# Optimization experiments

Hardware: AMD Instinct MI355X
Metric: run time of the kernel (lower is better)

The kernel has to match this reference:

```python
import jax, jax.numpy as jnp
import numpy as np

N = 50000
E = 800000
D = 128
EPS = 1e-5


def setup_inputs() -> dict:
    key = jax.random.key(0)
    ks = jax.random.split(key, 8)
    scale = 1.0 / np.sqrt(D)
    x = jax.random.normal(ks[0], (N, D), dtype=jnp.float32)
    edge_index = jax.random.randint(ks[1], (2, E), 0, N, dtype=jnp.int64)
    return {
        "x": x,
        "edge_index": edge_index,
        "W1l": jax.random.normal(ks[2], (D, D), dtype=jnp.float32) * scale,
        "b1": jnp.zeros((D,), jnp.float32),
        "W1r": jax.random.normal(ks[3], (D, D), dtype=jnp.float32) * scale,
        "g1": jnp.ones((D,), jnp.float32),
        "bt1": jnp.zeros((D,), jnp.float32),
        "W2l": jax.random.normal(ks[4], (D, D), dtype=jnp.float32) * scale,
        "b2": jnp.zeros((D,), jnp.float32),
        "W2r": jax.random.normal(ks[5], (D, D), dtype=jnp.float32) * scale,
        "g2": jnp.ones((D,), jnp.float32),
        "bt2": jnp.zeros((D,), jnp.float32),
    }


def _sage(x, src, dst, Wl, b, Wr):
    # mean aggregation of source features at destination nodes
    agg = jax.ops.segment_sum(x[src], dst, num_segments=N)  # [N, D]
    deg = jax.ops.segment_sum(jnp.ones((E,), x.dtype), dst, num_segments=N)
    agg = agg / jnp.maximum(deg, 1.0)[:, None]
    # PyG SAGEConv: lin_l(agg) + bias + lin_r(x) (root, no bias)
    return agg @ Wl + b + x @ Wr


def _bn(h, g, bt):
    # training-mode batch norm over node dim
    mu = jnp.mean(h, axis=0)
    var = jnp.var(h, axis=0)
    return (h - mu) * (g / jnp.sqrt(var + EPS)) + bt


def reference(x, edge_index, W1l, b1, W1r, g1, bt1, W2l, b2, W2r, g2, bt2):
    src, dst = edge_index[0], edge_index[1]
    h = _sage(x, src, dst, W1l, b1, W1r)
    h = jax.nn.relu(_bn(h, g1, bt1))
    # dropout = identity (eval mode)
    h = _sage(h, src, dst, W2l, b2, W2r)
    h = _bn(h, g2, bt2)
    # residual (in_channels == out_channels -> identity skip)
    return jax.nn.relu(h + x)
```

## Files before the change

kernel.cpp:

```cpp
#include <hip/hip_runtime.h>

typedef unsigned short u16;
typedef unsigned char u8;
typedef __attribute__((ext_vector_type(8))) short short8;
typedef __attribute__((ext_vector_type(2))) float f32x2;
typedef __attribute__((ext_vector_type(4))) float f32x4;
typedef __attribute__((ext_vector_type(4))) int i32x4;
typedef __attribute__((ext_vector_type(4))) unsigned short us4;
typedef __attribute__((ext_vector_type(8))) unsigned short us8;
typedef __attribute__((ext_vector_type(4))) unsigned int u32x4;

#define N_NODES 50000
#define N_EDGES 800000
#define DIM 128
#define NINV (1.0f / 50000.0f)
#define SROW 136
#define NBKT 3125
#define CAP 512
#define SUPN 800
#define NSUP 63
#define SEGCAP 16384

__device__ __forceinline__ float bf2f(u16 u) {
    union { unsigned int i; float f; } v; v.i = ((unsigned int)u) << 16; return v.f;
}
__device__ __forceinline__ u16 f2bf(float f) {
    union { float f; unsigned int i; } v; v.f = f;
    return (u16)((v.i + 0x7FFFu + ((v.i >> 16) & 1u)) >> 16);
}

__global__ __launch_bounds__(256) void k_prep(
        const float* __restrict__ W1l, const float* __restrict__ W1r, u16* __restrict__ Bp1,
        const float* __restrict__ W2l, const float* __restrict__ W2r, u16* __restrict__ Bp2,
        const float* __restrict__ x, u16* __restrict__ xh, u8* __restrict__ xf8,
        const int* __restrict__ esrc, const int* __restrict__ edst,
        int* __restrict__ segCnt, unsigned* __restrict__ segBuf, int splitB) {
    int b = blockIdx.x;
    if (b < 32) {
        const float* Wl = (b < 16) ? W1l : W2l;
        const float* Wr = (b < 16) ? W1r : W2r;
        u16* Bp = (b < 16) ? Bp1 : Bp2;
        int idx = (b & 15) * 256 + threadIdx.x;
        int lane = idx & 63;
        int kc = (idx >> 6) & 7;
        int nt = idx >> 9;
        int q = lane >> 4, nn = lane & 15;
        int col = nt * 16 + nn;
        #pragma unroll
        for (int j = 0; j < 8; ++j) {
            int k = kc * 32 + q * 8 + j;
            float v = (k < 128) ? Wl[k * 128 + col] : Wr[(k - 128) * 128 + col];
            Bp[(long)idx * 8 + j] = f2bf(v);
        }
    } else if (b < 32 + splitB) {
        long i4 = ((long)(b - 32) * 256 + threadIdx.x) * 4;
        f32x4 v = *(const f32x4*)(x + i4);
        us4 h;
        #pragma unroll
        for (int j = 0; j < 4; ++j) h[j] = f2bf(v[j]);
        *(us4*)(xh + i4) = h;
        int p = __builtin_amdgcn_cvt_pk_fp8_f32(v[0], v[1], 0, false);
        p = __builtin_amdgcn_cvt_pk_fp8_f32(v[2], v[3], p, true);
        *(int*)(xf8 + i4) = p;
    } else {
        __shared__ int sHistB[64], sScanB[64], sCurB[64], sBaseB[64];
        __shared__ unsigned sStage[1024];
        __shared__ u8 sBinOf[1024];
        int tid = threadIdx.x;
        int hb = b - 32 - splitB;
        int e4 = hb * 1024 + tid * 4;
        bool val = e4 < N_EDGES;
        if (tid < 64) sHistB[tid] = 0;
        __syncthreads();
        unsigned ent[4]; int bin[4];
        if (val) {
            i32x4 d4 = *(const i32x4*)(edst + e4);
            i32x4 s4 = *(const i32x4*)(esrc + e4);
            #pragma unroll
            for (int j = 0; j < 4; ++j) {
                unsigned dd = (unsigned)d4[j];
                int bi = (int)(dd / 800u);
                bin[j] = bi;
                ent[j] = ((unsigned)s4[j] << 10) | (dd - (unsigned)bi * 800u);
                atomicAdd(&sHistB[bi], 1);
            }
        }
        __syncthreads();
        if (tid == 0) {
            int acc = 0;
            #pragma unroll
            for (int i = 0; i < 64; ++i) { sScanB[i] = acc; sCurB[i] = acc; acc += sHistB[i]; }
        }
        __syncthreads();
        if (val) {
            #pragma unroll
            for (int j = 0; j < 4; ++j) {
                int p = atomicAdd(&sCurB[bin[j]], 1);
                sStage[p] = ent[j];
                sBinOf[p] = (u8)bin[j];
            }
        }
        __syncthreads();
        if (tid < 64) {
            int c = sHistB[tid];
            sBaseB[tid] = c ? atomicAdd(&segCnt[tid << 4], c) : 0;
        }
        __syncthreads();
        int tcount = sScanB[63] + sHistB[63];
        for (int p = tid; p < tcount; p += 256) {
            int bn = sBinOf[p];
            long ofs = (long)sBaseB[bn] + (p - sScanB[bn]);
            if (ofs < SEGCAP)
                segBuf[(long)bn * SEGCAP + ofs] = sStage[p];
        }
    }
}

__global__ __launch_bounds__(512) void k_sort(
        const int* __restrict__ segCnt, const unsigned* __restrict__ segBuf,
        u16* __restrict__ col_srt, u16* __restrict__ hdr) {
    __shared__ int sHist[SUPN], sStart[SUPN], sCur[SUPN];
    int tid = threadIdx.x;
    int s = blockIdx.x;
    int nnodes = N_NODES - s * SUPN; if (nnodes > SUPN) nnodes = SUPN;
    int ngroups = nnodes >> 4;
    int n = segCnt[s << 4]; if (n > SEGCAP) n = SEGCAP;
    for (int i = tid; i < SUPN; i += 512) { sHist[i] = 0; sCur[i] = 0; }
    __syncthreads();
    const unsigned* seg = segBuf + (long)s * SEGCAP;
    unsigned ent[32];
    #pragma unroll
    for (int i = 0; i < 32; ++i) {
        int idx = i * 512 + tid;
        ent[i] = (idx < n) ? seg[idx] : 0xFFFFFFFFu;
    }
    #pragma unroll
    for (int i = 0; i < 32; ++i)
        if (ent[i] != 0xFFFFFFFFu) atomicAdd(&sHist[ent[i] & 1023u], 1);
    __syncthreads();
    if (tid < ngroups) {
        int base = 0;
        int gb = (s * 50 + tid) * 32;
        #pragma unroll
        for (int i = 0; i < 16; ++i) {
            int node = tid * 16 + i;
            int d = sHist[node];
            int st_c = base < CAP ? base : CAP;
            int en_c = base + d < CAP ? base + d : CAP;
            sStart[node] = base;
            hdr[gb + i] = (u16)st_c;
            hdr[gb + 16 + i] = (u16)(en_c - st_c);
            base += d;
        }
    }
    __syncthreads();
    #pragma unroll
    for (int i = 0; i < 32; ++i) {
        unsigned e = ent[i];
        if (e != 0xFFFFFFFFu) {
            int node = (int)(e & 1023u);
            int pos = atomicAdd(&sCur[node], 1);
            int ofs = sStart[node] + pos;
            if (ofs < CAP)
                col_srt[(long)(s * 50 + (node >> 4)) * CAP + ofs] = (u16)(e >> 10);
        }
    }
}

template<int BN>
__device__ __forceinline__ void acc_row16(u32x4 w,
        float sum[16], const float av[16], const float ov[16]) {
    float t[16];
    f32x2 p;
    #pragma unroll
    for (int h = 0; h < 4; ++h) {
        p = __builtin_amdgcn_cvt_pk_f32_fp8((int)w[h], false); t[h*4+0] = p[0]; t[h*4+1] = p[1];
        p = __builtin_amdgcn_cvt_pk_f32_fp8((int)w[h], true);  t[h*4+2] = p[0]; t[h*4+3] = p[1];
    }
    #pragma unroll
    for (int k = 0; k < 16; ++k) {
        float v = t[k];
        if (BN) { v = v * av[k] + ov[k]; v = v > 0.f ? v : 0.f; }
        sum[k] += v;
    }
}

template<int BN, int W8>
__global__ __launch_bounds__(256) void k_ag(
        const u8* __restrict__ fq, const u16* __restrict__ fh,
        const u16* __restrict__ hdr, const u16* __restrict__ col_srt,
        const u16* __restrict__ Bph, const float* __restrict__ bias,
        const float* __restrict__ statsPrev, const float* __restrict__ gP,
        const float* __restrict__ btP,
        u16* __restrict__ h16, u8* __restrict__ h8, float* __restrict__ stats) {
    __shared__ u16 sA[16 * SROW];
    __shared__ float acS[256];
    __shared__ __align__(16) u16 sIdx[CAP];
    int tid = threadIdx.x;
    long nodebase = (long)blockIdx.x * 16;

    if (tid < 64)
        *(us8*)(sIdx + tid * 8) = *(const us8*)(col_srt + (long)blockIdx.x * CAP + tid * 8);

    if (BN) {
        if (tid < 128) {
            float s = 0.f, qq = 0.f;
            #pragma unroll
            for (int b = 0; b < 8; ++b) {
                s  += statsPrev[b * 512 + tid];
                qq += statsPrev[b * 512 + 256 + tid];
            }
            float mu = s * NINV;
            float var = qq * NINV - mu * mu;
            float a = gP[tid] * rsqrtf(var + 1e-5f);
            acS[tid] = a;
            acS[128 + tid] = btP[tid] - mu * a;
        }
    }
    __syncthreads();

    {
        int grp = tid >> 4;
        int g   = tid & 15;
        int sub = g >> 3;
        int gl  = g & 7;
        int d16 = gl * 16;
        int st  = hdr[blockIdx.x * 32 + grp];
        int deg = hdr[blockIdx.x * 32 + 16 + grp];
        int s = st, e = st + deg;
        float av[16], ov[16];
        if (BN) {
            #pragma unroll
            for (int k = 0; k < 16; ++k) { av[k] = acS[d16 + k]; ov[k] = acS[128 + d16 + k]; }
        }
        float sum[16];
        #pragma unroll
        for (int k = 0; k < 16; ++k) sum[k] = 0.f;
        int j = s + sub;
        for (; j + 6 < e; j += 8) {
            int i0 = sIdx[j], i1 = sIdx[j + 2], i2 = sIdx[j + 4], i3 = sIdx[j + 6];
            u32x4 w0 = *(const u32x4*)(fq + (long)i0 * DIM + d16);
            u32x4 w1 = *(const u32x4*)(fq + (long)i1 * DIM + d16);
            u32x4 w2 = *(const u32x4*)(fq + (long)i2 * DIM + d16);
            u32x4 w3 = *(const u32x4*)(fq + (long)i3 * DIM + d16);
            acc_row16<BN>(w0, sum, av, ov);
            acc_row16<BN>(w1, sum, av, ov);
            acc_row16<BN>(w2, sum, av, ov);
            acc_row16<BN>(w3, sum, av, ov);
        }
        for (; j < e; j += 2) {
            int i0 = sIdx[j];
            u32x4 w0 = *(const u32x4*)(fq + (long)i0 * DIM + d16);
            acc_row16<BN>(w0, sum, av, ov);
        }
        #pragma unroll
        for (int k = 0; k < 16; ++k) sum[k] += __shfl_xor(sum[k], 8);
        if (sub == 0) {
            float dn = (deg > 0) ? 1.f / (float)deg : 1.f;
            us8 r0, r1;
            #pragma unroll
            for (int k = 0; k < 8; ++k) {
                r0[k] = f2bf(sum[k] * dn);
                r1[k] = f2bf(sum[8 + k] * dn);
            }
            *(us8*)(sA + grp * SROW + d16) = r0;
            *(us8*)(sA + grp * SROW + d16 + 8) = r1;
        }
    }
    __syncthreads();

    int cg = tid >> 6, lane = tid & 63;
    int q = lane >> 4, nn = lane & 15;
    long rc = nodebase + nn;

    short8 ah[8];
    #pragma unroll
    for (int kc = 0; kc < 4; ++kc)
        ah[kc] = *(const short8*)(sA + nn * SROW + kc * 32 + q * 8);
    #pragma unroll
    for (int kc = 0; kc < 4; ++kc) {
        int ko = kc * 32 + q * 8;
        us8 rv = *(const us8*)(fh + rc * DIM + ko);
        short8 t;
        if (BN) {
            #pragma unroll
            for (int j = 0; j < 8; ++j) {
                float v = bf2f(rv[j]) * acS[ko + j] + acS[128 + ko + j];
                t[j] = (short)f2bf(v > 0.f ? v : 0.f);
            }
        } else {
            #pragma unroll
            for (int j = 0; j < 8; ++j) t[j] = (short)rv[j];
        }
        ah[4 + kc] = t;
    }

    f32x4 acc[2];
    acc[0] = (f32x4){0.f, 0.f, 0.f, 0.f};
    acc[1] = (f32x4){0.f, 0.f, 0.f, 0.f};

    #pragma unroll
    for (int kc = 0; kc < 8; ++kc) {
        #pragma unroll
        for (int nt = 0; nt < 2; ++nt) {
            int ntg = cg * 2 + nt;
            short8 bh = *(const short8*)(Bph + (((ntg * 8 + kc) * 64 + lane) << 3));
            acc[nt] = __builtin_amdgcn_mfma_f32_16x16x32_bf16(ah[kc], bh, acc[nt], 0, 0, 0);
        }
    }

    int bank = blockIdx.x & 7;
    #pragma unroll
    for (int nt = 0; nt < 2; ++nt) {
        int col = cg * 32 + nt * 16 + nn;
        float bv = bias[col];
        float ps = 0.f, pq = 0.f;
        #pragma unroll
        for (int r = 0; r < 4; ++r) {
            float v = acc[nt][r] + bv;
            long idx = (nodebase + q * 4 + r) * DIM + col;
            h16[idx] = f2bf(v);
            if (W8) {
                int pb = __builtin_amdgcn_cvt_pk_fp8_f32(v, v, 0, false);
                h8[idx] = (u8)(pb & 0xff);
            }
            ps += v; pq += v * v;
        }
        ps += __shfl_xor(ps, 16);
        ps += __shfl_xor(ps, 32);
        pq += __shfl_xor(pq, 16);
        pq += __shfl_xor(pq, 32);
        if (q == 0) {
            atomicAdd(&stats[bank * 512 + col], ps);
            atomicAdd(&stats[bank * 512 + 256 + col], pq);
        }
    }
}

__global__ __launch_bounds__(256) void k_bn_add_relu(
        const u16* __restrict__ h, const float* __restrict__ stats,
        const float* __restrict__ g, const float* __restrict__ bt,
        const float* __restrict__ x, float* __restrict__ outv) {
    __shared__ float acS[256];
    int tid = threadIdx.x;
    if (tid < 128) {
        float s = 0.f, qq = 0.f;
        #pragma unroll
        for (int b = 0; b < 8; ++b) {
            s  += stats[b * 512 + tid];
            qq += stats[b * 512 + 256 + tid];
        }
        float mu = s * NINV;
        float var = qq * NINV - mu * mu;
        float a = g[tid] * rsqrtf(var + 1e-5f);
        acS[tid] = a;
        acS[128 + tid] = bt[tid] - mu * a;
    }
    __syncthreads();
    long i8 = ((long)blockIdx.x * 256 + tid) * 8;
    int c = (int)(i8 & 127);
    us8 hv = *(const us8*)(h + i8);
    f32x4 x0 = *(const f32x4*)(x + i8);
    f32x4 x1 = *(const f32x4*)(x + i8 + 4);
    f32x4 r0, r1;
    #pragma unroll
    for (int j = 0; j < 4; ++j) {
        float v = bf2f(hv[j]) * acS[c + j] + acS[128 + c + j] + x0[j];
        r0[j] = v > 0.f ? v : 0.f;
        float w = bf2f(hv[4 + j]) * acS[c + 4 + j] + acS[128 + c + 4 + j] + x1[j];
        r1[j] = w > 0.f ? w : 0.f;
    }
    *(f32x4*)(outv + i8) = r0;
    *(f32x4*)(outv + i8 + 4) = r1;
}

extern "C" void kernel_launch(void* const* d_in, const int* in_sizes, int n_in,
                              void* d_out, int out_size, void* d_ws, size_t ws_size,
                              hipStream_t stream) {
    (void)in_sizes; (void)n_in; (void)out_size; (void)ws_size;
    const float* x   = (const float*)d_in[0];
    const int*   ei  = (const int*)d_in[1];
    const float* W1l = (const float*)d_in[2];
    const float* b1  = (const float*)d_in[3];
    const float* W1r = (const float*)d_in[4];
    const float* g1  = (const float*)d_in[5];
    const float* bt1 = (const float*)d_in[6];
    const float* W2l = (const float*)d_in[7];
    const float* b2  = (const float*)d_in[8];
    const float* W2r = (const float*)d_in[9];
    const float* g2  = (const float*)d_in[10];
    const float* bt2 = (const float*)d_in[11];
    float* out = (float*)d_out;

    const int* esrc = ei;
    const int* edst = ei + N_EDGES;

    char* ws = (char*)d_ws;
    size_t off = 0;
    auto alloc = [&](size_t bytes) { size_t p = off; off = (off + bytes + 255) & ~(size_t)255; return p; };
    float* stats1  = (float*)(ws + alloc(4096 * 4));
    float* stats2  = (float*)(ws + alloc(4096 * 4));
    int*   segCnt  = (int*)  (ws + alloc(64 * 16 * 4));
    size_t zero_bytes = off;
    unsigned* segBuf = (unsigned*)(ws + alloc((size_t)NSUP * SEGCAP * 4));
    u16*   col_srt = (u16*)  (ws + alloc((size_t)NBKT * CAP * 2));
    u16*   hdr     = (u16*)  (ws + alloc((size_t)NBKT * 32 * 2));
    u16*   xh      = (u16*)  (ws + alloc((size_t)N_NODES * DIM * 2));
    u8*    xf8     = (u8*)   (ws + alloc((size_t)N_NODES * DIM));
    u16*   hb1     = (u16*)  (ws + alloc((size_t)N_NODES * DIM * 2));
    u8*    h1f8    = (u8*)   (ws + alloc((size_t)N_NODES * DIM));
    u16*   hb2     = (u16*)  (ws + alloc((size_t)N_NODES * DIM * 2));
    u16*   Bp1h    = (u16*)  (ws + alloc(256 * 128 * 2));
    u16*   Bp2h    = (u16*)  (ws + alloc(256 * 128 * 2));

    hipMemsetAsync(ws, 0, zero_bytes, stream);

    const int AGB = N_NODES / 16;
    const int EWB4 = (int)(((long)N_NODES * DIM) / 1024);
    const int EWB8 = (int)(((long)N_NODES * DIM) / 2048);
    const int EDGB = (N_EDGES + 1023) / 1024;
    const int PREPB = 32 + EWB4 + EDGB;

    k_prep<<<PREPB, 256, 0, stream>>>(W1l, W1r, Bp1h, W2l, W2r, Bp2h, x, xh, xf8,
                                      esrc, edst, segCnt, segBuf, EWB4);

    k_sort<<<NSUP, 512, 0, stream>>>(segCnt, segBuf, col_srt, hdr);

    k_ag<0, 1><<<AGB, 256, 0, stream>>>(xf8, xh, hdr, col_srt, Bp1h, b1,
                                        stats1, g1, bt1, hb1, h1f8, stats1);

    k_ag<1, 0><<<AGB, 256, 0, stream>>>(h1f8, hb1, hdr, col_srt, Bp2h, b2,
                                        stats1, g1, bt1, hb2, h1f8, stats2);

    k_bn_add_relu<<<EWB8, 256, 0, stream>>>(hb2, stats2, g2, bt2, x, out);
}
```

Measured before the change: 207.1 us.

## Drop bf16 copy of x and deepen gather loop to eight rows

The prep kernel no longer writes a bf16 copy of x. It only writes the fp8 copy, now eight elements per thread. The first aggregation kernel instead reads x in fp32 and converts it to bf16 in registers for the root-term MFMA operand, which cuts one full-size write and later re-read of x. A new 16-edge gather loop also issues eight fp8 row loads before accumulating, to raise memory-level parallelism, at the cost of more registers.

```diff
diff --git a/kernel.cpp b/kernel.cpp
--- a/kernel.cpp
+++ b/kernel.cpp
@@ -6,6 +6,7 @@
 typedef __attribute__((ext_vector_type(2))) float f32x2;
 typedef __attribute__((ext_vector_type(4))) float f32x4;
 typedef __attribute__((ext_vector_type(4))) int i32x4;
+typedef __attribute__((ext_vector_type(2))) int i32x2;
 typedef __attribute__((ext_vector_type(4))) unsigned short us4;
 typedef __attribute__((ext_vector_type(8))) unsigned short us8;
 typedef __attribute__((ext_vector_type(4))) unsigned int u32x4;
@@ -32,7 +33,7 @@
 __global__ __launch_bounds__(256) void k_prep(
         const float* __restrict__ W1l, const float* __restrict__ W1r, u16* __restrict__ Bp1,
         const float* __restrict__ W2l, const float* __restrict__ W2r, u16* __restrict__ Bp2,
-        const float* __restrict__ x, u16* __restrict__ xh, u8* __restrict__ xf8,
+        const float* __restrict__ x, u8* __restrict__ xf8,
         const int* __restrict__ esrc, const int* __restrict__ edst,
         int* __restrict__ segCnt, unsigned* __restrict__ segBuf, int splitB) {
     int b = blockIdx.x;
@@ -53,15 +54,15 @@
             Bp[(long)idx * 8 + j] = f2bf(v);
         }
     } else if (b < 32 + splitB) {
-        long i4 = ((long)(b - 32) * 256 + threadIdx.x) * 4;
-        f32x4 v = *(const f32x4*)(x + i4);
-        us4 h;
-        #pragma unroll
-        for (int j = 0; j < 4; ++j) h[j] = f2bf(v[j]);
-        *(us4*)(xh + i4) = h;
-        int p = __builtin_amdgcn_cvt_pk_fp8_f32(v[0], v[1], 0, false);
-        p = __builtin_amdgcn_cvt_pk_fp8_f32(v[2], v[3], p, true);
-        *(int*)(xf8 + i4) = p;
+        long i8 = ((long)(b - 32) * 256 + threadIdx.x) * 8;
+        f32x4 v0 = *(const f32x4*)(x + i8);
+        f32x4 v1 = *(const f32x4*)(x + i8 + 4);
+        int p0 = __builtin_amdgcn_cvt_pk_fp8_f32(v0[0], v0[1], 0, false);
+        p0 = __builtin_amdgcn_cvt_pk_fp8_f32(v0[2], v0[3], p0, true);
+        int p1 = __builtin_amdgcn_cvt_pk_fp8_f32(v1[0], v1[1], 0, false);
+        p1 = __builtin_amdgcn_cvt_pk_fp8_f32(v1[2], v1[3], p1, true);
+        i32x2 pp; pp[0] = p0; pp[1] = p1;
+        *(i32x2*)(xf8 + i8) = pp;
     } else {
         __shared__ int sHistB[64], sScanB[64], sCurB[64], sBaseB[64];
         __shared__ unsigned sStage[1024];
@@ -185,9 +186,9 @@
     }
 }
 
-template<int BN, int W8>
+template<int BN, int W8, int XF32>
 __global__ __launch_bounds__(256) void k_ag(
-        const u8* __restrict__ fq, const u16* __restrict__ fh,
+        const u8* __restrict__ fq, const u16* __restrict__ fh, const float* __restrict__ xf,
         const u16* __restrict__ hdr, const u16* __restrict__ col_srt,
         const u16* __restrict__ Bph, const float* __restrict__ bias,
         const float* __restrict__ statsPrev, const float* __restrict__ gP,
@@ -237,6 +238,17 @@
         #pragma unroll
         for (int k = 0; k < 16; ++k) sum[k] = 0.f;
         int j = s + sub;
+        for (; j + 14 < e; j += 16) {
+            int ii[8];
+            #pragma unroll
+            for (int t8 = 0; t8 < 8; ++t8) ii[t8] = sIdx[j + 2 * t8];
+            u32x4 w[8];
+            #pragma unroll
+            for (int t8 = 0; t8 < 8; ++t8)
+                w[t8] = *(const u32x4*)(fq + (long)ii[t8] * DIM + d16);
+            #pragma unroll
+            for (int t8 = 0; t8 < 8; ++t8) acc_row16<BN>(w[t8], sum, av, ov);
+        }
         for (; j + 6 < e; j += 8) {
             int i0 = sIdx[j], i1 = sIdx[j + 2], i2 = sIdx[j + 4], i3 = sIdx[j + 6];
             u32x4 w0 = *(const u32x4*)(fq + (long)i0 * DIM + d16);
@@ -280,17 +292,27 @@
     #pragma unroll
     for (int kc = 0; kc < 4; ++kc) {
         int ko = kc * 32 + q * 8;
-        us8 rv = *(const us8*)(fh + rc * DIM + ko);
         short8 t;
-        if (BN) {
-            #pragma unroll
-            for (int j = 0; j < 8; ++j) {
-                float v = bf2f(rv[j]) * acS[ko + j] + acS[128 + ko + j];
-                t[j] = (short)f2bf(v > 0.f ? v : 0.f);
+        if (XF32) {
+            f32x4 v0 = *(const f32x4*)(xf + rc * DIM + ko);
+            f32x4 v1 = *(const f32x4*)(xf + rc * DIM + ko + 4);
+            #pragma unroll
+            for (int j = 0; j < 4; ++j) {
+                t[j] = (short)f2bf(v0[j]);
+                t[4 + j] = (short)f2bf(v1[j]);
             }
         } else {
-            #pragma unroll
-            for (int j = 0; j < 8; ++j) t[j] = (short)rv[j];
+            us8 rv = *(const us8*)(fh + rc * DIM + ko);
+            if (BN) {
+                #pragma unroll
+                for (int j = 0; j < 8; ++j) {
+                    float v = bf2f(rv[j]) * acS[ko + j] + acS[128 + ko + j];
+                    t[j] = (short)f2bf(v > 0.f ? v : 0.f);
+                }
+            } else {
+                #pragma unroll
+                for (int j = 0; j < 8; ++j) t[j] = (short)rv[j];
+            }
         }
         ah[4 + kc] = t;
     }
@@ -405,7 +427,6 @@
     unsigned* segBuf = (unsigned*)(ws + alloc((size_t)NSUP * SEGCAP * 4));
     u16*   col_srt = (u16*)  (ws + alloc((size_t)NBKT * CAP * 2));
     u16*   hdr     = (u16*)  (ws + alloc((size_t)NBKT * 32 * 2));
-    u16*   xh      = (u16*)  (ws + alloc((size_t)N_NODES * DIM * 2));
     u8*    xf8     = (u8*)   (ws + alloc((size_t)N_NODES * DIM));
     u16*   hb1     = (u16*)  (ws + alloc((size_t)N_NODES * DIM * 2));
     u8*    h1f8    = (u8*)   (ws + alloc((size_t)N_NODES * DIM));
@@ -416,21 +437,20 @@
     hipMemsetAsync(ws, 0, zero_bytes, stream);
 
     const int AGB = N_NODES / 16;
-    const int EWB4 = (int)(((long)N_NODES * DIM) / 1024);
     const int EWB8 = (int)(((long)N_NODES * DIM) / 2048);
     const int EDGB = (N_EDGES + 1023) / 1024;
-    const int PREPB = 32 + EWB4 + EDGB;
-
-    k_prep<<<PREPB, 256, 0, stream>>>(W1l, W1r, Bp1h, W2l, W2r, Bp2h, x, xh, xf8,
-                                      esrc, edst, segCnt, segBuf, EWB4);
+    const int PREPB = 32 + EWB8 + EDGB;
+
+    k_prep<<<PREPB, 256, 0, stream>>>(W1l, W1r, Bp1h, W2l, W2r, Bp2h, x, xf8,
+                                      esrc, edst, segCnt, segBuf, EWB8);
 
     k_sort<<<NSUP, 512, 0, stream>>>(segCnt, segBuf, col_srt, hdr);
 
-    k_ag<0, 1><<<AGB, 256, 0, stream>>>(xf8, xh, hdr, col_srt, Bp1h, b1,
-                                        stats1, g1, bt1, hb1, h1f8, stats1);
-
-    k_ag<1, 0><<<AGB, 256, 0, stream>>>(h1f8, hb1, hdr, col_srt, Bp2h, b2,
-                                        stats1, g1, bt1, hb2, h1f8, stats2);
+    k_ag<0, 1, 1><<<AGB, 256, 0, stream>>>(xf8, (const u16*)nullptr, x, hdr, col_srt,
+                                           Bp1h, b1, stats1, g1, bt1, hb1, h1f8, stats1);
+
+    k_ag<1, 0, 0><<<AGB, 256, 0, stream>>>(h1f8, hb1, (const float*)nullptr, hdr, col_srt,
+                                           Bp2h, b2, stats1, g1, bt1, hb2, h1f8, stats2);
 
     k_bn_add_relu<<<EWB8, 256, 0, stream>>>(hb2, stats2, g2, bt2, x, out);
 }
```

After: 222.4 us. +7.4%, slower.
